# Kernel tuning notes

Hardware: AMD Instinct MI355X
Metric: run time of the kernel (lower is better)

Reference implementation:

```python
import jax, jax.numpy as jnp
import numpy as np

NUM_NODES = 50000
NUM_EDGES = 800000
NUM_FEATURES = 128
HIDDEN = 128
NUM_GRAPHS = 256


def gcn_conv(x, W, b, src, dst, num_nodes):
    """PyG GCNConv: add self-loops, symmetric deg normalization, scatter-add, bias."""
    h = x @ W  # [N, H]
    # add self-loops
    loop = jnp.arange(num_nodes, dtype=src.dtype)
    src_f = jnp.concatenate([src, loop])
    dst_f = jnp.concatenate([dst, loop])
    # degree of destination nodes (includes self-loops)
    deg = jax.ops.segment_sum(jnp.ones_like(dst_f, dtype=h.dtype), dst_f,
                              num_segments=num_nodes)
    dinv = jnp.where(deg > 0, jax.lax.rsqrt(deg), 0.0)
    norm = dinv[src_f] * dinv[dst_f]  # [E+N]
    msg = h[src_f] * norm[:, None]    # gather + scale
    out = jax.ops.segment_sum(msg, dst_f, num_segments=num_nodes)
    return out + b


def global_mean_pool(x, batch, num_graphs):
    s = jax.ops.segment_sum(x, batch, num_segments=num_graphs)
    cnt = jax.ops.segment_sum(jnp.ones((x.shape[0],), dtype=x.dtype), batch,
                              num_segments=num_graphs)
    return s / jnp.maximum(cnt, 1.0)[:, None]


def setup_inputs() -> dict:
    key = jax.random.key(0)
    ks = jax.random.split(key, 8)
    x = jax.random.normal(ks[0], (NUM_NODES, NUM_FEATURES), dtype=jnp.float32)
    edge_index = jax.random.randint(ks[1], (2, NUM_EDGES), 0, NUM_NODES, dtype=jnp.int64)
    batch = jax.random.randint(ks[2], (NUM_NODES,), 0, NUM_GRAPHS, dtype=jnp.int64)
    # glorot-ish init for weights
    s1 = 1.0 / np.sqrt(NUM_FEATURES)
    s2 = 1.0 / np.sqrt(HIDDEN)
    W1 = jax.random.normal(ks[3], (NUM_FEATURES, HIDDEN), dtype=jnp.float32) * s1
    b1 = jnp.zeros((HIDDEN,), dtype=jnp.float32)
    W2 = jax.random.normal(ks[4], (HIDDEN, HIDDEN), dtype=jnp.float32) * s2
    b2 = jnp.zeros((HIDDEN,), dtype=jnp.float32)
    lin_W = jax.random.normal(ks[5], (HIDDEN, 1), dtype=jnp.float32) * s2
    lin_b = jnp.zeros((1,), dtype=jnp.float32)
    return {"x": x, "edge_index": edge_index, "batch": batch,
            "W1": W1, "b1": b1, "W2": W2, "b2": b2,
            "lin_W": lin_W, "lin_b": lin_b}


def reference(x, edge_index, batch, W1, b1, W2, b2, lin_W, lin_b):
    src, dst = edge_index[0], edge_index[1]
    n = x.shape[0]
    h = jax.nn.relu(gcn_conv(x, W1, b1, src, dst, n))
    h = jax.nn.relu(gcn_conv(h, W2, b2, src, dst, n))
    g = global_mean_pool(h, batch, NUM_GRAPHS)  # [G, H]
    return g @ lin_W + lin_b                    # [G, 1]
```

## Files before the change

### kernel.cpp

```cpp
#include <hip/hip_runtime.h>

#define NFEAT 128
#define NPART 64
#define NAUX  128
#define CAP   64

typedef unsigned int uint;
typedef __attribute__((ext_vector_type(8))) short short8v;
typedef __attribute__((ext_vector_type(8))) unsigned short ushort8v;
typedef __attribute__((ext_vector_type(4))) float floatx4;

__device__ inline float bf2f(unsigned short u) {
    return __uint_as_float(((uint)u) << 16);
}
__device__ inline unsigned short f2bf(float f) {
    uint u = __float_as_uint(f);
    return (unsigned short)((u + 0x7fffu + ((u >> 16) & 1u)) >> 16);
}

__global__ __launch_bounds__(256) void zero_kernel(int4* __restrict__ p, int n4) {
    int i = blockIdx.x * 256 + threadIdx.x;
    int stride = gridDim.x * 256;
    int4 z = make_int4(0, 0, 0, 0);
    for (; i < n4; i += stride) p[i] = z;
}

__global__ void prep_kernel(const int* __restrict__ src, const int* __restrict__ dst,
                            const int* __restrict__ batch,
                            const float* __restrict__ W1, const float* __restrict__ W2,
                            int* __restrict__ cnt, unsigned short* __restrict__ csr,
                            unsigned short* __restrict__ wt, float* __restrict__ gcntp,
                            int E, int N) {
    if (blockIdx.x < 4096) {
        const int shard = blockIdx.x & 7;
        const int blk = blockIdx.x >> 3;
        const int span = (N + 7) >> 3;
        const int lo = shard * span;
        const int hi = min(N, lo + span);
        const int stride = 512 * 256;
        for (int e = blk * 256 + (int)threadIdx.x; e < E; e += stride) {
            int d = __builtin_nontemporal_load(dst + e);
            if (d >= lo && d < hi) {
                int pos = atomicAdd(&cnt[d], 1);
                if (pos < CAP)
                    csr[d * CAP + pos] = (unsigned short)__builtin_nontemporal_load(src + e);
            }
        }
    } else {
        const int ab = blockIdx.x - 4096;
        const int tid = threadIdx.x;
        const int idx = ab * 256 + tid;
        {
            const float* W = (idx < 16384) ? W1 : W2;
            int i = idx & 16383;
            int k = i >> 7, n = i & 127;
            float v = W[k * 128 + n];
            unsigned short h = f2bf(v);
            unsigned short l = f2bf(v - bf2f(h));
            int nt = n >> 4, nl = n & 15;
            int kc = k >> 5, kg = (k >> 3) & 3, j = k & 7;
            int fpos = ((kc * 8 + nt) * 64 + kg * 16 + nl) * 8 + j;
            unsigned short* base = wt + (idx < 16384 ? 0 : 2) * 16384;
            base[fpos] = h;
            base[16384 + fpos] = l;
        }
        __shared__ int hist[256];
        hist[tid] = 0;
        __syncthreads();
        const int per = (N + NAUX - 1) / NAUX;
        const int lo2 = ab * per;
        const int hi2 = min(N, lo2 + per);
        for (int v = lo2 + tid; v < hi2; v += 256) atomicAdd(&hist[batch[v]], 1);
        __syncthreads();
        gcntp[ab * 256 + tid] = (float)hist[tid];
    }
}

__global__ __launch_bounds__(256) void gemm1_mfma_kernel(const float* __restrict__ X,
                                                         const unsigned short* __restrict__ wt,
                                                         const int* __restrict__ cnt,
                                                         unsigned short* __restrict__ out,
                                                         int nrows) {
    __shared__ unsigned short xs_hi[64][72], xs_lo[64][72];
    const int tid = threadIdx.x;
    const int w = tid >> 6, lane = tid & 63;
    const int nl = lane & 15, kg = lane >> 4;
    const int row0 = blockIdx.x * 64;

    floatx4 acc[8];
#pragma unroll
    for (int nt = 0; nt < 8; ++nt) acc[nt] = (floatx4){0.f, 0.f, 0.f, 0.f};

    for (int p = 0; p < 2; ++p) {
        __syncthreads();
        for (int idx = tid; idx < 64 * 16; idx += 256) {
            int r = idx >> 4, q = idx & 15;
            float4 v = make_float4(0.f, 0.f, 0.f, 0.f);
            if (row0 + r < nrows)
                v = ((const float4*)(X + (size_t)(row0 + r) * NFEAT + p * 64))[q];
            ushort4 h, l;
            h.x = f2bf(v.x); l.x = f2bf(v.x - bf2f(h.x));
            h.y = f2bf(v.y); l.y = f2bf(v.y - bf2f(h.y));
            h.z = f2bf(v.z); l.z = f2bf(v.z - bf2f(h.z));
            h.w = f2bf(v.w); l.w = f2bf(v.w - bf2f(h.w));
            *(ushort4*)&xs_hi[r][q * 4] = h;
            *(ushort4*)&xs_lo[r][q * 4] = l;
        }
        __syncthreads();
#pragma unroll
        for (int kc = 0; kc < 2; ++kc) {
            const int k8 = kc * 32 + kg * 8;
            const int kcg = p * 2 + kc;
            short8v ah = *(const short8v*)&xs_hi[w * 16 + nl][k8];
            short8v al = *(const short8v*)&xs_lo[w * 16 + nl][k8];
#pragma unroll
            for (int nt = 0; nt < 8; ++nt) {
                const size_t fo = (size_t)((kcg * 8 + nt) * 64 + lane) * 8;
                short8v bh = *(const short8v*)(wt + fo);
                short8v bl = *(const short8v*)(wt + 16384 + fo);
                acc[nt] = __builtin_amdgcn_mfma_f32_16x16x32_bf16(ah, bh, acc[nt], 0, 0, 0);
                acc[nt] = __builtin_amdgcn_mfma_f32_16x16x32_bf16(al, bh, acc[nt], 0, 0, 0);
                acc[nt] = __builtin_amdgcn_mfma_f32_16x16x32_bf16(ah, bl, acc[nt], 0, 0, 0);
            }
        }
    }
    const int rbase = row0 + w * 16 + kg * 4;
#pragma unroll
    for (int reg = 0; reg < 4; ++reg) {
        int grow = rbase + reg;
        if (grow < nrows) {
            float dv = rsqrtf((float)(cnt[grow] + 1));
#pragma unroll
            for (int nt = 0; nt < 8; ++nt)
                out[(size_t)grow * NFEAT + nt * 16 + nl] = f2bf(acc[nt][reg] * dv);
        }
    }
}

__global__ __launch_bounds__(256) void gemm2_mfma_kernel(const unsigned short* __restrict__ X,
                                                         const unsigned short* __restrict__ wt,
                                                         const int* __restrict__ cnt,
                                                         unsigned short* __restrict__ out,
                                                         int nrows) {
    __shared__ unsigned short xs[64][72];
    const int tid = threadIdx.x;
    const int w = tid >> 6, lane = tid & 63;
    const int nl = lane & 15, kg = lane >> 4;
    const int row0 = blockIdx.x * 64;

    floatx4 acc[8];
#pragma unroll
    for (int nt = 0; nt < 8; ++nt) acc[nt] = (floatx4){0.f, 0.f, 0.f, 0.f};

    for (int p = 0; p < 2; ++p) {
        __syncthreads();
        for (int idx = tid; idx < 64 * 8; idx += 256) {
            int r = idx >> 3, q = idx & 7;
            short8v v = {0, 0, 0, 0, 0, 0, 0, 0};
            if (row0 + r < nrows)
                v = *(const short8v*)(X + (size_t)(row0 + r) * NFEAT + p * 64 + q * 8);
            *(short8v*)&xs[r][q * 8] = v;
        }
        __syncthreads();
#pragma unroll
        for (int kc = 0; kc < 2; ++kc) {
            const int k8 = kc * 32 + kg * 8;
            const int kcg = p * 2 + kc;
            short8v a = *(const short8v*)&xs[w * 16 + nl][k8];
#pragma unroll
            for (int nt = 0; nt < 8; ++nt) {
                const size_t fo = (size_t)((kcg * 8 + nt) * 64 + lane) * 8;
                short8v bh = *(const short8v*)(wt + fo);
                short8v bl = *(const short8v*)(wt + 16384 + fo);
                acc[nt] = __builtin_amdgcn_mfma_f32_16x16x32_bf16(a, bh, acc[nt], 0, 0, 0);
                acc[nt] = __builtin_amdgcn_mfma_f32_16x16x32_bf16(a, bl, acc[nt], 0, 0, 0);
            }
        }
    }
    const int rbase = row0 + w * 16 + kg * 4;
#pragma unroll
    for (int reg = 0; reg < 4; ++reg) {
        int grow = rbase + reg;
        if (grow < nrows) {
            float dv = rsqrtf((float)(cnt[grow] + 1));
#pragma unroll
            for (int nt = 0; nt < 8; ++nt)
                out[(size_t)grow * NFEAT + nt * 16 + nl] = f2bf(acc[nt][reg] * dv);
        }
    }
}

__device__ inline void agg_gather8(const ushort8v* __restrict__ hp8,
                                   const unsigned short* __restrict__ csr,
                                   int v, int d, int ep, int q, float acc[8]) {
    const int s = v * CAP;
    if (ep == 0) {
        ushort8v r = hp8[(size_t)v * 16 + q];
#pragma unroll
        for (int k = 0; k < 8; ++k) acc[k] += bf2f(r[k]);
    }
    int i = 0;
    for (; i + 16 <= d; i += 16) {
        int u[4];
#pragma unroll
        for (int j = 0; j < 4; ++j) u[j] = csr[s + i + 4 * j + ep];
        ushort8v a[4];
#pragma unroll
        for (int j = 0; j < 4; ++j) a[j] = hp8[(size_t)u[j] * 16 + q];
#pragma unroll
        for (int j = 0; j < 4; ++j)
#pragma unroll
            for (int k = 0; k < 8; ++k) acc[k] += bf2f(a[j][k]);
    }
    if (i < d) {
        int u[4];
#pragma unroll
        for (int j = 0; j < 4; ++j) {
            int e = i + 4 * j + ep;
            u[j] = csr[s + (e < d ? e : d - 1)];
        }
        ushort8v a[4];
#pragma unroll
        for (int j = 0; j < 4; ++j) a[j] = hp8[(size_t)u[j] * 16 + q];
#pragma unroll
        for (int j = 0; j < 4; ++j) {
            if (i + 4 * j + ep < d) {
#pragma unroll
                for (int k = 0; k < 8; ++k) acc[k] += bf2f(a[j][k]);
            }
        }
    }
#pragma unroll
    for (int k = 0; k < 8; ++k) {
        acc[k] += __shfl_xor(acc[k], 16);
        acc[k] += __shfl_xor(acc[k], 32);
    }
}

__global__ __launch_bounds__(256) void agg_relu_kernel(const ushort8v* __restrict__ hp8,
                                                       const int* __restrict__ cnt,
                                                       const unsigned short* __restrict__ csr,
                                                       const float* __restrict__ bias,
                                                       unsigned short* __restrict__ out,
                                                       int N, int npw) {
    const int wgl = (blockIdx.x * 256 + threadIdx.x) >> 6;
    const int lane = threadIdx.x & 63;
    const int ep = lane >> 4;
    const int q = lane & 15;
    float4 bb0 = *(const float4*)(bias + q * 8);
    float4 bb1 = *(const float4*)(bias + q * 8 + 4);
    const int v0 = wgl * npw;
    const int v1 = min(N, v0 + npw);
    for (int v = v0; v < v1; ++v) {
        int d = cnt[v];
        float acc[8] = {0, 0, 0, 0, 0, 0, 0, 0};
        agg_gather8(hp8, csr, v, d, ep, q, acc);
        if (ep == 0) {
            const float dv = rsqrtf((float)(d + 1));
            ushort8v o;
            o[0] = f2bf(fmaxf(fmaf(acc[0], dv, bb0.x), 0.f));
            o[1] = f2bf(fmaxf(fmaf(acc[1], dv, bb0.y), 0.f));
            o[2] = f2bf(fmaxf(fmaf(acc[2], dv, bb0.z), 0.f));
            o[3] = f2bf(fmaxf(fmaf(acc[3], dv, bb0.w), 0.f));
            o[4] = f2bf(fmaxf(fmaf(acc[4], dv, bb1.x), 0.f));
            o[5] = f2bf(fmaxf(fmaf(acc[5], dv, bb1.y), 0.f));
            o[6] = f2bf(fmaxf(fmaf(acc[6], dv, bb1.z), 0.f));
            o[7] = f2bf(fmaxf(fmaf(acc[7], dv, bb1.w), 0.f));
            *(ushort8v*)(out + (size_t)v * NFEAT + q * 8) = o;
        }
    }
}

__global__ __launch_bounds__(256) void agg_pool_kernel(const ushort8v* __restrict__ hp8,
                                                       const int* __restrict__ cnt,
                                                       const unsigned short* __restrict__ csr,
                                                       const float* __restrict__ bias,
                                                       const float* __restrict__ linW,
                                                       const int* __restrict__ batch,
                                                       float* __restrict__ gpart,
                                                       int N, int npw) {
    const int wgl = (blockIdx.x * 256 + threadIdx.x) >> 6;
    const int lane = threadIdx.x & 63;
    const int ep = lane >> 4;
    const int q = lane & 15;
    float4 bb0 = *(const float4*)(bias + q * 8);
    float4 bb1 = *(const float4*)(bias + q * 8 + 4);
    float4 lw0 = *(const float4*)(linW + q * 8);
    float4 lw1 = *(const float4*)(linW + q * 8 + 4);
    const int v0 = wgl * npw;
    const int v1 = min(N, v0 + npw);
    for (int v = v0; v < v1; ++v) {
        int d = cnt[v];
        float acc[8] = {0, 0, 0, 0, 0, 0, 0, 0};
        agg_gather8(hp8, csr, v, d, ep, q, acc);
        const float dv = rsqrtf((float)(d + 1));
        float sc = fmaxf(fmaf(acc[0], dv, bb0.x), 0.f) * lw0.x
                 + fmaxf(fmaf(acc[1], dv, bb0.y), 0.f) * lw0.y
                 + fmaxf(fmaf(acc[2], dv, bb0.z), 0.f) * lw0.z
                 + fmaxf(fmaf(acc[3], dv, bb0.w), 0.f) * lw0.w
                 + fmaxf(fmaf(acc[4], dv, bb1.x), 0.f) * lw1.x
                 + fmaxf(fmaf(acc[5], dv, bb1.y), 0.f) * lw1.y
                 + fmaxf(fmaf(acc[6], dv, bb1.z), 0.f) * lw1.z
                 + fmaxf(fmaf(acc[7], dv, bb1.w), 0.f) * lw1.w;
        sc += __shfl_xor(sc, 1);
        sc += __shfl_xor(sc, 2);
        sc += __shfl_xor(sc, 4);
        sc += __shfl_xor(sc, 8);
        if (lane == 0) atomicAdd(&gpart[(v & (NPART - 1)) * 256 + batch[v]], sc);
    }
}

__global__ void finalize_kernel(const float* __restrict__ gpart, const float* __restrict__ gcntp,
                                const float* __restrict__ linb, float* __restrict__ out, int G) {
    int g = threadIdx.x;
    if (g < G) {
        float s = 0.f;
        for (int p = 0; p < NPART; ++p) s += gpart[p * 256 + g];
        float c = 0.f;
        for (int b = 0; b < NAUX; ++b) c += gcntp[b * 256 + g];
        out[g] = s / fmaxf(c, 1.0f) + linb[0];
    }
}

extern "C" void kernel_launch(void* const* d_in, const int* in_sizes, int n_in,
                              void* d_out, int out_size, void* d_ws, size_t ws_size,
                              hipStream_t stream) {
    const float* x    = (const float*)d_in[0];
    const int*   eidx = (const int*)d_in[1];
    const int*   batch= (const int*)d_in[2];
    const float* W1   = (const float*)d_in[3];
    const float* b1   = (const float*)d_in[4];
    const float* W2   = (const float*)d_in[5];
    const float* b2   = (const float*)d_in[6];
    const float* linW = (const float*)d_in[7];
    const float* linb = (const float*)d_in[8];
    float* out = (float*)d_out;

    const int N = in_sizes[0] / NFEAT;
    const int E = in_sizes[1] / 2;
    const int G = out_size;
    const int* src = eidx;
    const int* dst = eidx + E;

    char* p = (char*)d_ws;
    unsigned short* hpBf  = (unsigned short*)p; p += (size_t)N * NFEAT * sizeof(unsigned short);
    unsigned short* h1Bf  = (unsigned short*)p; p += (size_t)N * NFEAT * sizeof(unsigned short);
    unsigned short* csr   = (unsigned short*)p; p += (size_t)N * CAP * sizeof(unsigned short);
    unsigned short* wt    = (unsigned short*)p; p += (size_t)4 * 16384 * sizeof(unsigned short);
    int*   cnt   = (int*)p;   p += (size_t)N * sizeof(int);
    float* gpart = (float*)p; p += (size_t)NPART * 256 * sizeof(float);
    float* gcntp = (float*)p; p += (size_t)NAUX * 256 * sizeof(float);
    (void)ws_size; (void)n_in;

    const int nz4 = (int)(((size_t)(N + NPART * 256) * 4 + 15) / 16);
    zero_kernel<<<256, 256, 0, stream>>>((int4*)cnt, nz4);

    prep_kernel<<<4096 + NAUX, 256, 0, stream>>>(src, dst, batch, W1, W2, cnt, csr, wt,
                                                 gcntp, E, N);

    const int NWAVE = 2048 * 4;
    const int npw = (N + NWAVE - 1) / NWAVE;

    gemm1_mfma_kernel<<<(N + 63) / 64, 256, 0, stream>>>(x, wt, cnt, hpBf, N);
    agg_relu_kernel<<<2048, 256, 0, stream>>>((const ushort8v*)hpBf, cnt, csr,
                                              b1, h1Bf, N, npw);
    gemm2_mfma_kernel<<<(N + 63) / 64, 256, 0, stream>>>(h1Bf, wt + 2 * 16384, cnt, hpBf, N);
    agg_pool_kernel<<<2048, 256, 0, stream>>>((const ushort8v*)hpBf, cnt, csr,
                                              b2, linW, batch, gpart, N, npw);
    finalize_kernel<<<1, 256, 0, stream>>>(gpart, gcntp, linb, out, G);
}
```

Before: 153.4 us.

## Overlap first GEMM with CSR build; apply source normalization during gather

The zeroing, weight-packing and batch-histogram work now runs in one small init kernel. The first GEMM runs inside the CSR-building prep kernel as extra blocks, so the two independent phases execute concurrently and one launch disappears. Because the GEMM no longer waits for degree counts, it stores unscaled features, and the first aggregation applies each neighbor's rsqrt(degree) per edge. This adds a cnt lookup and an rsqrt per gathered edge in layer 1.

Measured after the change: 166.2 us. 8.3% more time.

```diff
diff --git a/kernel.cpp b/kernel.cpp
--- a/kernel.cpp
+++ b/kernel.cpp
@@ -18,22 +18,108 @@
     return (unsigned short)((u + 0x7fffu + ((u >> 16) & 1u)) >> 16);
 }
 
-__global__ __launch_bounds__(256) void zero_kernel(int4* __restrict__ p, int n4) {
-    int i = blockIdx.x * 256 + threadIdx.x;
-    int stride = gridDim.x * 256;
+__global__ __launch_bounds__(256) void init_kernel(const float* __restrict__ W1,
+                                                   const float* __restrict__ W2,
+                                                   const int* __restrict__ batch,
+                                                   unsigned short* __restrict__ wt,
+                                                   float* __restrict__ gcntp,
+                                                   int4* __restrict__ zbase, int nz4, int N) {
+    const int ab = blockIdx.x;
+    const int tid = threadIdx.x;
+    const int idx = ab * 256 + tid;
     int4 z = make_int4(0, 0, 0, 0);
-    for (; i < n4; i += stride) p[i] = z;
-}
-
-__global__ void prep_kernel(const int* __restrict__ src, const int* __restrict__ dst,
-                            const int* __restrict__ batch,
-                            const float* __restrict__ W1, const float* __restrict__ W2,
-                            int* __restrict__ cnt, unsigned short* __restrict__ csr,
-                            unsigned short* __restrict__ wt, float* __restrict__ gcntp,
-                            int E, int N) {
-    if (blockIdx.x < 4096) {
-        const int shard = blockIdx.x & 7;
-        const int blk = blockIdx.x >> 3;
+    for (int i = idx; i < nz4; i += NAUX * 256) zbase[i] = z;
+    {
+        const float* W = (idx < 16384) ? W1 : W2;
+        int i = idx & 16383;
+        int k = i >> 7, n = i & 127;
+        float v = W[k * 128 + n];
+        unsigned short h = f2bf(v);
+        unsigned short l = f2bf(v - bf2f(h));
+        int nt = n >> 4, nl = n & 15;
+        int kc = k >> 5, kg = (k >> 3) & 3, j = k & 7;
+        int fpos = ((kc * 8 + nt) * 64 + kg * 16 + nl) * 8 + j;
+        unsigned short* base = wt + (idx < 16384 ? 0 : 2) * 16384;
+        base[fpos] = h;
+        base[16384 + fpos] = l;
+    }
+    __shared__ int hist[256];
+    hist[tid] = 0;
+    __syncthreads();
+    const int per = (N + NAUX - 1) / NAUX;
+    const int lo2 = ab * per;
+    const int hi2 = min(N, lo2 + per);
+    for (int v = lo2 + tid; v < hi2; v += 256) atomicAdd(&hist[batch[v]], 1);
+    __syncthreads();
+    gcntp[ab * 256 + tid] = (float)hist[tid];
+}
+
+__global__ __launch_bounds__(256) void prep_kernel(const int* __restrict__ src,
+                                                   const int* __restrict__ dst,
+                                                   const float* __restrict__ X,
+                                                   const unsigned short* __restrict__ wt,
+                                                   int* __restrict__ cnt,
+                                                   unsigned short* __restrict__ csr,
+                                                   unsigned short* __restrict__ hpBf,
+                                                   int E, int N, int ng1) {
+    if ((int)blockIdx.x < ng1) {
+        __shared__ unsigned short xs_hi[64][72], xs_lo[64][72];
+        const int tid = threadIdx.x;
+        const int w = tid >> 6, lane = tid & 63;
+        const int nl = lane & 15, kg = lane >> 4;
+        const int row0 = blockIdx.x * 64;
+
+        floatx4 acc[8];
+#pragma unroll
+        for (int nt = 0; nt < 8; ++nt) acc[nt] = (floatx4){0.f, 0.f, 0.f, 0.f};
+
+        for (int p = 0; p < 2; ++p) {
+            __syncthreads();
+            for (int idx = tid; idx < 64 * 16; idx += 256) {
+                int r = idx >> 4, q = idx & 15;
+                float4 v = make_float4(0.f, 0.f, 0.f, 0.f);
+                if (row0 + r < N)
+                    v = ((const float4*)(X + (size_t)(row0 + r) * NFEAT + p * 64))[q];
+                ushort4 h, l;
+                h.x = f2bf(v.x); l.x = f2bf(v.x - bf2f(h.x));
+                h.y = f2bf(v.y); l.y = f2bf(v.y - bf2f(h.y));
+                h.z = f2bf(v.z); l.z = f2bf(v.z - bf2f(h.z));
+                h.w = f2bf(v.w); l.w = f2bf(v.w - bf2f(h.w));
+                *(ushort4*)&xs_hi[r][q * 4] = h;
+                *(ushort4*)&xs_lo[r][q * 4] = l;
+            }
+            __syncthreads();
+#pragma unroll
+            for (int kc = 0; kc < 2; ++kc) {
+                const int k8 = kc * 32 + kg * 8;
+                const int kcg = p * 2 + kc;
+                short8v ah = *(const short8v*)&xs_hi[w * 16 + nl][k8];
+                short8v al = *(const short8v*)&xs_lo[w * 16 + nl][k8];
+#pragma unroll
+                for (int nt = 0; nt < 8; ++nt) {
+                    const size_t fo = (size_t)((kcg * 8 + nt) * 64 + lane) * 8;
+                    short8v bh = *(const short8v*)(wt + fo);
+                    short8v bl = *(const short8v*)(wt + 16384 + fo);
+                    acc[nt] = __builtin_amdgcn_mfma_f32_16x16x32_bf16(ah, bh, acc[nt], 0, 0, 0);
+                    acc[nt] = __builtin_amdgcn_mfma_f32_16x16x32_bf16(al, bh, acc[nt], 0, 0, 0);
+                    acc[nt] = __builtin_amdgcn_mfma_f32_16x16x32_bf16(ah, bl, acc[nt], 0, 0, 0);
+                }
+            }
+        }
+        const int rbase = row0 + w * 16 + kg * 4;
+#pragma unroll
+        for (int reg = 0; reg < 4; ++reg) {
+            int grow = rbase + reg;
+            if (grow < N) {
+#pragma unroll
+                for (int nt = 0; nt < 8; ++nt)
+                    hpBf[(size_t)grow * NFEAT + nt * 16 + nl] = f2bf(acc[nt][reg]);
+            }
+        }
+    } else {
+        const int b = (int)blockIdx.x - ng1;
+        const int shard = b & 7;
+        const int blk = b >> 3;
         const int span = (N + 7) >> 3;
         const int lo = shard * span;
         const int hi = min(N, lo + span);
@@ -46,94 +132,6 @@
                     csr[d * CAP + pos] = (unsigned short)__builtin_nontemporal_load(src + e);
             }
         }
-    } else {
-        const int ab = blockIdx.x - 4096;
-        const int tid = threadIdx.x;
-        const int idx = ab * 256 + tid;
-        {
-            const float* W = (idx < 16384) ? W1 : W2;
-            int i = idx & 16383;
-            int k = i >> 7, n = i & 127;
-            float v = W[k * 128 + n];
-            unsigned short h = f2bf(v);
-            unsigned short l = f2bf(v - bf2f(h));
-            int nt = n >> 4, nl = n & 15;
-            int kc = k >> 5, kg = (k >> 3) & 3, j = k & 7;
-            int fpos = ((kc * 8 + nt) * 64 + kg * 16 + nl) * 8 + j;
-            unsigned short* base = wt + (idx < 16384 ? 0 : 2) * 16384;
-            base[fpos] = h;
-            base[16384 + fpos] = l;
-        }
-        __shared__ int hist[256];
-        hist[tid] = 0;
-        __syncthreads();
-        const int per = (N + NAUX - 1) / NAUX;
-        const int lo2 = ab * per;
-        const int hi2 = min(N, lo2 + per);
-        for (int v = lo2 + tid; v < hi2; v += 256) atomicAdd(&hist[batch[v]], 1);
-        __syncthreads();
-        gcntp[ab * 256 + tid] = (float)hist[tid];
-    }
-}
-
-__global__ __launch_bounds__(256) void gemm1_mfma_kernel(const float* __restrict__ X,
-                                                         const unsigned short* __restrict__ wt,
-                                                         const int* __restrict__ cnt,
-                                                         unsigned short* __restrict__ out,
-                                                         int nrows) {
-    __shared__ unsigned short xs_hi[64][72], xs_lo[64][72];
-    const int tid = threadIdx.x;
-    const int w = tid >> 6, lane = tid & 63;
-    const int nl = lane & 15, kg = lane >> 4;
-    const int row0 = blockIdx.x * 64;
-
-    floatx4 acc[8];
-#pragma unroll
-    for (int nt = 0; nt < 8; ++nt) acc[nt] = (floatx4){0.f, 0.f, 0.f, 0.f};
-
-    for (int p = 0; p < 2; ++p) {
-        __syncthreads();
-        for (int idx = tid; idx < 64 * 16; idx += 256) {
-            int r = idx >> 4, q = idx & 15;
-            float4 v = make_float4(0.f, 0.f, 0.f, 0.f);
-            if (row0 + r < nrows)
-                v = ((const float4*)(X + (size_t)(row0 + r) * NFEAT + p * 64))[q];
-            ushort4 h, l;
-            h.x = f2bf(v.x); l.x = f2bf(v.x - bf2f(h.x));
-            h.y = f2bf(v.y); l.y = f2bf(v.y - bf2f(h.y));
-            h.z = f2bf(v.z); l.z = f2bf(v.z - bf2f(h.z));
-            h.w = f2bf(v.w); l.w = f2bf(v.w - bf2f(h.w));
-            *(ushort4*)&xs_hi[r][q * 4] = h;
-            *(ushort4*)&xs_lo[r][q * 4] = l;
-        }
-        __syncthreads();
-#pragma unroll
-        for (int kc = 0; kc < 2; ++kc) {
-            const int k8 = kc * 32 + kg * 8;
-            const int kcg = p * 2 + kc;
-            short8v ah = *(const short8v*)&xs_hi[w * 16 + nl][k8];
-            short8v al = *(const short8v*)&xs_lo[w * 16 + nl][k8];
-#pragma unroll
-            for (int nt = 0; nt < 8; ++nt) {
-                const size_t fo = (size_t)((kcg * 8 + nt) * 64 + lane) * 8;
-                short8v bh = *(const short8v*)(wt + fo);
-                short8v bl = *(const short8v*)(wt + 16384 + fo);
-                acc[nt] = __builtin_amdgcn_mfma_f32_16x16x32_bf16(ah, bh, acc[nt], 0, 0, 0);
-                acc[nt] = __builtin_amdgcn_mfma_f32_16x16x32_bf16(al, bh, acc[nt], 0, 0, 0);
-                acc[nt] = __builtin_amdgcn_mfma_f32_16x16x32_bf16(ah, bl, acc[nt], 0, 0, 0);
-            }
-        }
-    }
-    const int rbase = row0 + w * 16 + kg * 4;
-#pragma unroll
-    for (int reg = 0; reg < 4; ++reg) {
-        int grow = rbase + reg;
-        if (grow < nrows) {
-            float dv = rsqrtf((float)(cnt[grow] + 1));
-#pragma unroll
-            for (int nt = 0; nt < 8; ++nt)
-                out[(size_t)grow * NFEAT + nt * 16 + nl] = f2bf(acc[nt][reg] * dv);
-        }
     }
 }
 
@@ -187,6 +185,61 @@
             for (int nt = 0; nt < 8; ++nt)
                 out[(size_t)grow * NFEAT + nt * 16 + nl] = f2bf(acc[nt][reg] * dv);
         }
+    }
+}
+
+__device__ inline void agg_gather8s(const ushort8v* __restrict__ hp8,
+                                    const int* __restrict__ cnt,
+                                    const unsigned short* __restrict__ csr,
+                                    int v, int d, int ep, int q, float acc[8]) {
+    const int s = v * CAP;
+    if (ep == 0) {
+        float dvv = rsqrtf((float)(d + 1));
+        ushort8v r = hp8[(size_t)v * 16 + q];
+#pragma unroll
+        for (int k = 0; k < 8; ++k) acc[k] = fmaf(bf2f(r[k]), dvv, acc[k]);
+    }
+    int i = 0;
+    for (; i + 16 <= d; i += 16) {
+        int u[4];
+#pragma unroll
+        for (int j = 0; j < 4; ++j) u[j] = csr[s + i + 4 * j + ep];
+        float dvu[4];
+#pragma unroll
+        for (int j = 0; j < 4; ++j) dvu[j] = rsqrtf((float)(cnt[u[j]] + 1));
+        ushort8v a[4];
+#pragma unroll
+        for (int j = 0; j < 4; ++j) a[j] = hp8[(size_t)u[j] * 16 + q];
+#pragma unroll
+        for (int j = 0; j < 4; ++j)
+#pragma unroll
+            for (int k = 0; k < 8; ++k) acc[k] = fmaf(bf2f(a[j][k]), dvu[j], acc[k]);
+    }
+    if (i < d) {
+        int u[4];
+#pragma unroll
+        for (int j = 0; j < 4; ++j) {
+            int e = i + 4 * j + ep;
+            u[j] = csr[s + (e < d ? e : d - 1)];
+        }
+        float dvu[4];
+#pragma unroll
+        for (int j = 0; j < 4; ++j) dvu[j] = rsqrtf((float)(cnt[u[j]] + 1));
+        ushort8v a[4];
+#pragma unroll
+        for (int j = 0; j < 4; ++j) a[j] = hp8[(size_t)u[j] * 16 + q];
+#pragma unroll
+        for (int j = 0; j < 4; ++j) {
+            if (i + 4 * j + ep < d) {
+#pragma unroll
+                for (int k = 0; k < 8; ++k) acc[k] = fmaf(bf2f(a[j][k]), dvu[j], acc[k]);
+            }
+        }
+    }
+#pragma unroll
+    for (int k = 0; k < 8; ++k) {
+        acc[k] += __shfl_xor(acc[k], 16);
+        acc[k] += __shfl_xor(acc[k], 32);
     }
 }
 
@@ -254,7 +307,7 @@
     for (int v = v0; v < v1; ++v) {
         int d = cnt[v];
         float acc[8] = {0, 0, 0, 0, 0, 0, 0, 0};
-        agg_gather8(hp8, csr, v, d, ep, q, acc);
+        agg_gather8s(hp8, cnt, csr, v, d, ep, q, acc);
         if (ep == 0) {
             const float dv = rsqrtf((float)(d + 1));
             ushort8v o;
@@ -341,6 +394,7 @@
     const int G = out_size;
     const int* src = eidx;
     const int* dst = eidx + E;
+    const int NG1 = (N + 63) / 64;
 
     char* p = (char*)d_ws;
     unsigned short* hpBf  = (unsigned short*)p; p += (size_t)N * NFEAT * sizeof(unsigned short);
@@ -353,15 +407,14 @@
     (void)ws_size; (void)n_in;
 
     const int nz4 = (int)(((size_t)(N + NPART * 256) * 4 + 15) / 16);
-    zero_kernel<<<256, 256, 0, stream>>>((int4*)cnt, nz4);
-
-    prep_kernel<<<4096 + NAUX, 256, 0, stream>>>(src, dst, batch, W1, W2, cnt, csr, wt,
-                                                 gcntp, E, N);
+
+    init_kernel<<<NAUX, 256, 0, stream>>>(W1, W2, batch, wt, gcntp, (int4*)cnt, nz4, N);
+
+    prep_kernel<<<NG1 + 4096, 256, 0, stream>>>(src, dst, x, wt, cnt, csr, hpBf, E, N, NG1);
 
     const int NWAVE = 2048 * 4;
     const int npw = (N + NWAVE - 1) / NWAVE;
 
-    gemm1_mfma_kernel<<<(N + 63) / 64, 256, 0, stream>>>(x, wt, cnt, hpBf, N);
     agg_relu_kernel<<<2048, 256, 0, stream>>>((const ushort8v*)hpBf, cnt, csr,
                                               b1, h1Bf, N, npw);
     gemm2_mfma_kernel<<<(N + 63) / 64, 256, 0, stream>>>(h1Bf, wt + 2 * 16384, cnt, hpBf, N);
```
